# Performance work log

Measured on AMD Instinct MI355X. Metric: run time of the kernel, lower is better.

## Reference

```python
import jax, jax.numpy as jnp
import numpy as np

N = 8192
EPS = 1e-6


def setup_inputs() -> dict:
    key = jax.random.key(0)
    k1, k2, k3, k4 = jax.random.split(key, 4)
    P_risk = jax.random.normal(k1, (N,), dtype=jnp.float32)
    P_surv = jax.random.normal(k2, (N,), dtype=jnp.float32)
    T = jax.random.uniform(k3, (N,), dtype=jnp.float32)
    E = jax.random.randint(k4, (N,), 0, 2, dtype=jnp.int32)
    return {"P_risk": P_risk, "P_surv": P_surv, "T": T, "E": E}


def _compute_loss(P, M, E_eff):
    # P: [N] log-hazards, M: [N, N] float mask, E_eff: [N] effective event weights
    P_exp = jnp.exp(P)
    # sum_j M[i, j] * exp(P[j])  -- masked risk-set sum as a matvec
    P_exp_sum = M @ P_exp
    log_ratio = jnp.log(P_exp / (P_exp_sum + EPS))
    return -jnp.sum(log_ratio * E_eff) / jnp.sum(E_eff)


def reference(P_risk, P_surv, T, E):
    Ef = E.astype(jnp.float32)
    # M_risk[i, j] = 1 if T[i] < T[j]
    M_risk = (T[:, None] < T[None, :]).astype(jnp.float32)
    # M_surv[i, j] = 1 if T[i] > T[j] and E[j] == 1
    M_surv = (T[:, None] > T[None, :]).astype(jnp.float32) * Ef[None, :]

    # mode='risk': E * (row of M_risk nonempty)
    E_risk = Ef * (jnp.sum(M_risk, axis=1) > 0).astype(jnp.float32)
    # mode='surv': just (row of M_surv nonempty)
    E_surv = (jnp.sum(M_surv, axis=1) > 0).astype(jnp.float32)

    loss_risk = _compute_loss(P_risk, M_risk, E_risk)
    loss_surv = _compute_loss(P_surv, M_surv, E_surv)
    return (loss_risk, loss_surv)
```

## Files before the change

kernel.cpp:

```cpp
#include <hip/hip_runtime.h>
#include <math.h>

#define NN   8192
#define R    8
#define HALF (NN / 2)
#define GX   ((NN / R) * 2)

#define EPSF 1e-6f


__global__ __launch_bounds__(256, 8) void ds_main(
    const float* __restrict__ Pr, const float* __restrict__ Ps,
    const float* __restrict__ T,  const int* __restrict__ E,
    float* __restrict__ sumR0, float* __restrict__ sumR1,
    float* __restrict__ sumS0, float* __restrict__ sumS1) {
  const int tid   = threadIdx.x;
  const int g     = blockIdx.x >> 1;
  const int h     = blockIdx.x & 1;
  const int row0  = g * R;
  const int jbase = h * HALF;

  float Ti[R];
#pragma unroll
  for (int r = 0; r < R; ++r) Ti[r] = T[row0 + r];

  float sr[R], ss[R];
#pragma unroll
  for (int r = 0; r < R; ++r) { sr[r] = 0.0f; ss[r] = 0.0f; }

  for (int k = 0; k < HALF; k += 1024) {
    const int j = jbase + k + tid * 4;
    float4 t4  = *(const float4*)(T  + j);
    float4 pr4 = *(const float4*)(Pr + j);
    float4 ps4 = *(const float4*)(Ps + j);
    int4   e4  = *(const int4*)(E  + j);
    float er0 = __expf(pr4.x), er1 = __expf(pr4.y),
          er2 = __expf(pr4.z), er3 = __expf(pr4.w);
    float es0 = e4.x ? __expf(ps4.x) : 0.0f;
    float es1 = e4.y ? __expf(ps4.y) : 0.0f;
    float es2 = e4.z ? __expf(ps4.z) : 0.0f;
    float es3 = e4.w ? __expf(ps4.w) : 0.0f;
#pragma unroll
    for (int r = 0; r < R; ++r) {
      bool g0 = t4.x > Ti[r];  sr[r] += g0 ? er0 : 0.0f;  ss[r] += g0 ? 0.0f : es0;
      bool g1 = t4.y > Ti[r];  sr[r] += g1 ? er1 : 0.0f;  ss[r] += g1 ? 0.0f : es1;
      bool g2 = t4.z > Ti[r];  sr[r] += g2 ? er2 : 0.0f;  ss[r] += g2 ? 0.0f : es2;
      bool g3 = t4.w > Ti[r];  sr[r] += g3 ? er3 : 0.0f;  ss[r] += g3 ? 0.0f : es3;
    }
  }

#pragma unroll
  for (int r = 0; r < R; ++r) {
    for (int off = 32; off > 0; off >>= 1) {
      sr[r] += __shfl_down(sr[r], off);
      ss[r] += __shfl_down(ss[r], off);
    }
  }
  __shared__ float sh[4][2 * R];
  const int wid = tid >> 6, lane = tid & 63;
  if (lane == 0) {
#pragma unroll
    for (int r = 0; r < R; ++r) { sh[wid][r] = sr[r]; sh[wid][R + r] = ss[r]; }
  }
  __syncthreads();
  if (tid < 2 * R) {
    float v = sh[0][tid] + sh[1][tid] + sh[2][tid] + sh[3][tid];
    float* SR = h ? sumR1 : sumR0;
    float* SS = h ? sumS1 : sumS0;
    if (tid < R) SR[row0 + tid] = v;
    else         SS[row0 + (tid - R)] = v;
  }
}

__global__ __launch_bounds__(1024) void ds_finalize(
    const float* __restrict__ Pr, const float* __restrict__ Ps,
    const int* __restrict__ E,
    const float* __restrict__ sumR0, const float* __restrict__ sumR1,
    const float* __restrict__ sumS0, const float* __restrict__ sumS1,
    float* __restrict__ out) {
  float nr = 0.0f, dr = 0.0f, ns = 0.0f, nds = 0.0f;
  for (int i = threadIdx.x; i < NN; i += 1024) {
    const int e = E[i];
    const float prv = Pr[i], psv = Ps[i];
    const float es_diag = e ? __expf(psv) : 0.0f;
    const float srv = sumR0[i] + sumR1[i];
    const float ssv = (sumS0[i] + sumS1[i]) - es_diag;
    const float wr  = (e != 0 && srv > 0.0f) ? 1.0f : 0.0f;
    const float wsv = (ssv > 0.0f) ? 1.0f : 0.0f;
    nr  += wr  * (prv - logf(srv + EPSF));
    dr  += wr;
    ns  += wsv * (psv - logf(ssv + EPSF));
    nds += wsv;
  }
  for (int off = 32; off > 0; off >>= 1) {
    nr  += __shfl_down(nr,  off);
    dr  += __shfl_down(dr,  off);
    ns  += __shfl_down(ns,  off);
    nds += __shfl_down(nds, off);
  }
  __shared__ float sh[4][16];
  const int wid = threadIdx.x >> 6, lane = threadIdx.x & 63;
  if (lane == 0) {
    sh[0][wid] = nr; sh[1][wid] = dr; sh[2][wid] = ns; sh[3][wid] = nds;
  }
  __syncthreads();
  if (threadIdx.x == 0) {
    float NR = 0, DR = 0, NS = 0, DS = 0;
#pragma unroll
    for (int w = 0; w < 16; ++w) {
      NR += sh[0][w]; DR += sh[1][w]; NS += sh[2][w]; DS += sh[3][w];
    }
    out[0] = -NR / DR;
    out[1] = -NS / DS;
  }
}

extern "C" void kernel_launch(void* const* d_in, const int* in_sizes, int n_in,
                              void* d_out, int out_size, void* d_ws, size_t ws_size,
                              hipStream_t stream) {
  const float* Pr = (const float*)d_in[0];
  const float* Ps = (const float*)d_in[1];
  const float* T  = (const float*)d_in[2];
  const int*   E  = (const int*)d_in[3];
  float* out = (float*)d_out;

  float* ws    = (float*)d_ws;
  float* sumR0 = ws;
  float* sumR1 = ws + NN;
  float* sumS0 = ws + 2 * NN;
  float* sumS1 = ws + 3 * NN;

  ds_main<<<GX, 256, 0, stream>>>(Pr, Ps, T, E, sumR0, sumR1, sumS0, sumS1);
  ds_finalize<<<1, 1024, 0, stream>>>(Pr, Ps, E, sumR0, sumR1, sumS0, sumS1, out);
}
```

Before: 75.96 us.

## Precompute packed exp values in bf16 with a prep kernel, drop the column split

Adds a prep kernel that computes exp(P_risk) and the E-masked exp(P_surv) once per element and packs them as two bf16 values next to T in an 8-byte record. The main kernel then reads one packed stream per column instead of four arrays and no longer recomputes exponentials for every row block. The grid is also changed from two half-column blocks per row group to one full-column block, which removes the partial-sum merge. This adds a kernel launch and rounds the exponentials to bf16, which loses precision in the risk-set sums.

Measured after the change: 76.47 us. Within noise of the previous version (+0.7%).

```diff
diff --git a/kernel.cpp b/kernel.cpp
--- a/kernel.cpp
+++ b/kernel.cpp
@@ -3,22 +3,33 @@
 
 #define NN   8192
 #define R    8
-#define HALF (NN / 2)
-#define GX   ((NN / R) * 2)
-
+#define GX   (NN / R)
 #define EPSF 1e-6f
 
 
-__global__ __launch_bounds__(256, 8) void ds_main(
+__device__ __forceinline__ unsigned bf16_rne(float x) {
+  unsigned u = __float_as_uint(x);
+  u += 0x7fffu + ((u >> 16) & 1u);
+  return u >> 16;
+}
+
+__global__ __launch_bounds__(256) void ds_prep(
     const float* __restrict__ Pr, const float* __restrict__ Ps,
     const float* __restrict__ T,  const int* __restrict__ E,
-    float* __restrict__ sumR0, float* __restrict__ sumR1,
-    float* __restrict__ sumS0, float* __restrict__ sumS1) {
-  const int tid   = threadIdx.x;
-  const int g     = blockIdx.x >> 1;
-  const int h     = blockIdx.x & 1;
-  const int row0  = g * R;
-  const int jbase = h * HALF;
+    uint2* __restrict__ pack2) {
+  int i = blockIdx.x * 256 + threadIdx.x;
+  float t  = T[i];
+  float er = __expf(Pr[i]);
+  float es = E[i] ? __expf(Ps[i]) : 0.0f;
+  unsigned c = bf16_rne(er) | (bf16_rne(es) << 16);
+  pack2[i] = make_uint2(__float_as_uint(t), c);
+}
+
+__global__ __launch_bounds__(256, 4) void ds_main(
+    const float* __restrict__ T, const int4* __restrict__ pack2,
+    float* __restrict__ sumR, float* __restrict__ sumS) {
+  const int tid  = threadIdx.x;
+  const int row0 = blockIdx.x * R;
 
   float Ti[R];
 #pragma unroll
@@ -28,24 +39,31 @@
 #pragma unroll
   for (int r = 0; r < R; ++r) { sr[r] = 0.0f; ss[r] = 0.0f; }
 
-  for (int k = 0; k < HALF; k += 1024) {
-    const int j = jbase + k + tid * 4;
-    float4 t4  = *(const float4*)(T  + j);
-    float4 pr4 = *(const float4*)(Pr + j);
-    float4 ps4 = *(const float4*)(Ps + j);
-    int4   e4  = *(const int4*)(E  + j);
-    float er0 = __expf(pr4.x), er1 = __expf(pr4.y),
-          er2 = __expf(pr4.z), er3 = __expf(pr4.w);
-    float es0 = e4.x ? __expf(ps4.x) : 0.0f;
-    float es1 = e4.y ? __expf(ps4.y) : 0.0f;
-    float es2 = e4.z ? __expf(ps4.z) : 0.0f;
-    float es3 = e4.w ? __expf(ps4.w) : 0.0f;
 #pragma unroll
-    for (int r = 0; r < R; ++r) {
-      bool g0 = t4.x > Ti[r];  sr[r] += g0 ? er0 : 0.0f;  ss[r] += g0 ? 0.0f : es0;
-      bool g1 = t4.y > Ti[r];  sr[r] += g1 ? er1 : 0.0f;  ss[r] += g1 ? 0.0f : es1;
-      bool g2 = t4.z > Ti[r];  sr[r] += g2 ? er2 : 0.0f;  ss[r] += g2 ? 0.0f : es2;
-      bool g3 = t4.w > Ti[r];  sr[r] += g3 ? er3 : 0.0f;  ss[r] += g3 ? 0.0f : es3;
+  for (int it = 0; it < 4; ++it) {
+    const int m = it * 1024 + tid;
+    int4 q0 = pack2[m];
+    int4 q1 = pack2[m + 256];
+    int4 q2 = pack2[m + 512];
+    int4 q3 = pack2[m + 768];
+#pragma unroll
+    for (int q = 0; q < 4; ++q) {
+      int4 p = (q == 0) ? q0 : (q == 1) ? q1 : (q == 2) ? q2 : q3;
+      float    t0 = __int_as_float(p.x);
+      unsigned c0 = (unsigned)p.y;
+      float    er0 = __uint_as_float(c0 << 16);
+      float    es0 = __uint_as_float(c0 & 0xffff0000u);
+      float    t1 = __int_as_float(p.z);
+      unsigned c1 = (unsigned)p.w;
+      float    er1 = __uint_as_float(c1 << 16);
+      float    es1 = __uint_as_float(c1 & 0xffff0000u);
+#pragma unroll
+      for (int r = 0; r < R; ++r) {
+        bool g0 = t0 > Ti[r];
+        sr[r] += g0 ? er0 : 0.0f;   ss[r] += g0 ? 0.0f : es0;
+        bool g1 = t1 > Ti[r];
+        sr[r] += g1 ? er1 : 0.0f;   ss[r] += g1 ? 0.0f : es1;
+      }
     }
   }
 
@@ -65,26 +83,23 @@
   __syncthreads();
   if (tid < 2 * R) {
     float v = sh[0][tid] + sh[1][tid] + sh[2][tid] + sh[3][tid];
-    float* SR = h ? sumR1 : sumR0;
-    float* SS = h ? sumS1 : sumS0;
-    if (tid < R) SR[row0 + tid] = v;
-    else         SS[row0 + (tid - R)] = v;
+    if (tid < R) sumR[row0 + tid] = v;
+    else         sumS[row0 + (tid - R)] = v;
   }
 }
 
 __global__ __launch_bounds__(1024) void ds_finalize(
     const float* __restrict__ Pr, const float* __restrict__ Ps,
-    const int* __restrict__ E,
-    const float* __restrict__ sumR0, const float* __restrict__ sumR1,
-    const float* __restrict__ sumS0, const float* __restrict__ sumS1,
+    const int* __restrict__ E,    const uint2* __restrict__ pack2,
+    const float* __restrict__ sumR, const float* __restrict__ sumS,
     float* __restrict__ out) {
   float nr = 0.0f, dr = 0.0f, ns = 0.0f, nds = 0.0f;
   for (int i = threadIdx.x; i < NN; i += 1024) {
     const int e = E[i];
     const float prv = Pr[i], psv = Ps[i];
-    const float es_diag = e ? __expf(psv) : 0.0f;
-    const float srv = sumR0[i] + sumR1[i];
-    const float ssv = (sumS0[i] + sumS1[i]) - es_diag;
+    const float es_diag = __uint_as_float(pack2[i].y & 0xffff0000u);
+    const float srv = sumR[i];
+    const float ssv = sumS[i] - es_diag;
     const float wr  = (e != 0 && srv > 0.0f) ? 1.0f : 0.0f;
     const float wsv = (ssv > 0.0f) ? 1.0f : 0.0f;
     nr  += wr  * (prv - logf(srv + EPSF));
@@ -124,12 +139,12 @@
   const int*   E  = (const int*)d_in[3];
   float* out = (float*)d_out;
 
-  float* ws    = (float*)d_ws;
-  float* sumR0 = ws;
-  float* sumR1 = ws + NN;
-  float* sumS0 = ws + 2 * NN;
-  float* sumS1 = ws + 3 * NN;
+  char*  ws    = (char*)d_ws;
+  uint2* pack2 = (uint2*)ws;
+  float* sumR  = (float*)(ws + (size_t)NN * sizeof(uint2));
+  float* sumS  = sumR + NN;
 
-  ds_main<<<GX, 256, 0, stream>>>(Pr, Ps, T, E, sumR0, sumR1, sumS0, sumS1);
-  ds_finalize<<<1, 1024, 0, stream>>>(Pr, Ps, E, sumR0, sumR1, sumS0, sumS1, out);
+  ds_prep<<<NN / 256, 256, 0, stream>>>(Pr, Ps, T, E, pack2);
+  ds_main<<<GX, 256, 0, stream>>>(T, (const int4*)pack2, sumR, sumS);
+  ds_finalize<<<1, 1024, 0, stream>>>(Pr, Ps, E, pack2, sumR, sumS, out);
 }
```

## Compute masks with scaled med3 clamp, derive surv sum by complement, drop column split

Applied to the files above, without the earlier changes.

The compare-and-select masks are replaced by a med3 clamp of the scaled time difference (T*2^30), so each mask costs a subtract plus med3 and feeds FMA accumulation. The survival sum is now the total event-weighted exp sum minus the accumulated above-threshold part, with clamping to zero in finalize. The column halving across blocks is removed: each block covers all columns with software-prefetched float4 loads and a per-wave staggered start, and the launch bound drops from 8 to 4 blocks per CU. Risks include the clamp being exactly 0 or 1 only when time differences exceed 2^-30, cancellation error in the complement subtraction, and half as many blocks to fill the GPU.

New measurement: 86.29 us. 13.6% more time.

```diff
diff --git a/kernel.cpp b/kernel.cpp
--- a/kernel.cpp
+++ b/kernel.cpp
@@ -3,88 +3,108 @@
 
 #define NN   8192
 #define R    8
-#define HALF (NN / 2)
-#define GX   ((NN / R) * 2)
-
+#define GX   (NN / R)
 #define EPSF 1e-6f
+#define BIGF 1073741824.0f
 
 
-__global__ __launch_bounds__(256, 8) void ds_main(
+__global__ __launch_bounds__(256, 4) void ds_main(
     const float* __restrict__ Pr, const float* __restrict__ Ps,
     const float* __restrict__ T,  const int* __restrict__ E,
-    float* __restrict__ sumR0, float* __restrict__ sumR1,
-    float* __restrict__ sumS0, float* __restrict__ sumS1) {
-  const int tid   = threadIdx.x;
-  const int g     = blockIdx.x >> 1;
-  const int h     = blockIdx.x & 1;
-  const int row0  = g * R;
-  const int jbase = h * HALF;
+    float* __restrict__ sumR, float* __restrict__ sumS) {
+  const int tid  = threadIdx.x;
+  const int wid  = tid >> 6, lane = tid & 63;
+  const int row0 = blockIdx.x * R;
 
-  float Ti[R];
+  float TiB[R];
 #pragma unroll
-  for (int r = 0; r < R; ++r) Ti[r] = T[row0 + r];
+  for (int r = 0; r < R; ++r) TiB[r] = T[row0 + r] * BIGF;
 
-  float sr[R], ss[R];
+  float sr[R], sa[R];
 #pragma unroll
-  for (int r = 0; r < R; ++r) { sr[r] = 0.0f; ss[r] = 0.0f; }
+  for (int r = 0; r < R; ++r) { sr[r] = 0.0f; sa[r] = 0.0f; }
+  float tot = 0.0f;
 
-  for (int k = 0; k < HALF; k += 1024) {
-    const int j = jbase + k + tid * 4;
-    float4 t4  = *(const float4*)(T  + j);
-    float4 pr4 = *(const float4*)(Pr + j);
-    float4 ps4 = *(const float4*)(Ps + j);
-    int4   e4  = *(const int4*)(E  + j);
-    float er0 = __expf(pr4.x), er1 = __expf(pr4.y),
-          er2 = __expf(pr4.z), er3 = __expf(pr4.w);
-    float es0 = e4.x ? __expf(ps4.x) : 0.0f;
-    float es1 = e4.y ? __expf(ps4.y) : 0.0f;
-    float es2 = e4.z ? __expf(ps4.z) : 0.0f;
-    float es3 = e4.w ? __expf(ps4.w) : 0.0f;
+  const float4* T4  = (const float4*)T;
+  const float4* Pr4 = (const float4*)Pr;
+  const float4* Ps4 = (const float4*)Ps;
+  const int4*   E4  = (const int4*)E;
+
+  const int c0 = (2 * wid) & 7;
+  int m = c0 * 256 + tid;
+  float4 t4 = T4[m], pr4 = Pr4[m], ps4 = Ps4[m];
+  int4   e4 = E4[m];
+
+#pragma unroll
+  for (int it = 0; it < 8; ++it) {
+    const int cn = (it + 1 + 2 * wid) & 7;
+    const int mn = cn * 256 + tid;
+    float4 t4n = T4[mn], pr4n = Pr4[mn], ps4n = Ps4[mn];
+    int4   e4n = E4[mn];
+
+    const float tB0 = t4.x * BIGF, tB1 = t4.y * BIGF,
+                tB2 = t4.z * BIGF, tB3 = t4.w * BIGF;
+    const float er0 = __expf(pr4.x), er1 = __expf(pr4.y),
+                er2 = __expf(pr4.z), er3 = __expf(pr4.w);
+    const float es0 = e4.x ? __expf(ps4.x) : 0.0f;
+    const float es1 = e4.y ? __expf(ps4.y) : 0.0f;
+    const float es2 = e4.z ? __expf(ps4.z) : 0.0f;
+    const float es3 = e4.w ? __expf(ps4.w) : 0.0f;
+    tot += (es0 + es1) + (es2 + es3);
+
 #pragma unroll
     for (int r = 0; r < R; ++r) {
-      bool g0 = t4.x > Ti[r];  sr[r] += g0 ? er0 : 0.0f;  ss[r] += g0 ? 0.0f : es0;
-      bool g1 = t4.y > Ti[r];  sr[r] += g1 ? er1 : 0.0f;  ss[r] += g1 ? 0.0f : es1;
-      bool g2 = t4.z > Ti[r];  sr[r] += g2 ? er2 : 0.0f;  ss[r] += g2 ? 0.0f : es2;
-      bool g3 = t4.w > Ti[r];  sr[r] += g3 ? er3 : 0.0f;  ss[r] += g3 ? 0.0f : es3;
+      const float m0 = __builtin_amdgcn_fmed3f(tB0 - TiB[r], 0.0f, 1.0f);
+      const float m1 = __builtin_amdgcn_fmed3f(tB1 - TiB[r], 0.0f, 1.0f);
+      const float m2 = __builtin_amdgcn_fmed3f(tB2 - TiB[r], 0.0f, 1.0f);
+      const float m3 = __builtin_amdgcn_fmed3f(tB3 - TiB[r], 0.0f, 1.0f);
+      sr[r] = fmaf(m0, er0, sr[r]);  sa[r] = fmaf(m0, es0, sa[r]);
+      sr[r] = fmaf(m1, er1, sr[r]);  sa[r] = fmaf(m1, es1, sa[r]);
+      sr[r] = fmaf(m2, er2, sr[r]);  sa[r] = fmaf(m2, es2, sa[r]);
+      sr[r] = fmaf(m3, er3, sr[r]);  sa[r] = fmaf(m3, es3, sa[r]);
     }
+    t4 = t4n; pr4 = pr4n; ps4 = ps4n; e4 = e4n;
   }
 
 #pragma unroll
   for (int r = 0; r < R; ++r) {
     for (int off = 32; off > 0; off >>= 1) {
       sr[r] += __shfl_down(sr[r], off);
-      ss[r] += __shfl_down(ss[r], off);
+      sa[r] += __shfl_down(sa[r], off);
     }
   }
-  __shared__ float sh[4][2 * R];
-  const int wid = tid >> 6, lane = tid & 63;
+  for (int off = 32; off > 0; off >>= 1) tot += __shfl_down(tot, off);
+
+  __shared__ float sh[4][2 * R + 1];
   if (lane == 0) {
 #pragma unroll
-    for (int r = 0; r < R; ++r) { sh[wid][r] = sr[r]; sh[wid][R + r] = ss[r]; }
+    for (int r = 0; r < R; ++r) { sh[wid][r] = sr[r]; sh[wid][R + r] = sa[r]; }
+    sh[wid][2 * R] = tot;
   }
   __syncthreads();
   if (tid < 2 * R) {
-    float v = sh[0][tid] + sh[1][tid] + sh[2][tid] + sh[3][tid];
-    float* SR = h ? sumR1 : sumR0;
-    float* SS = h ? sumS1 : sumS0;
-    if (tid < R) SR[row0 + tid] = v;
-    else         SS[row0 + (tid - R)] = v;
+    const float v  = sh[0][tid] + sh[1][tid] + sh[2][tid] + sh[3][tid];
+    if (tid < R) {
+      sumR[row0 + tid] = v;
+    } else {
+      const float tT = sh[0][2 * R] + sh[1][2 * R] + sh[2][2 * R] + sh[3][2 * R];
+      sumS[row0 + (tid - R)] = tT - v;
+    }
   }
 }
 
 __global__ __launch_bounds__(1024) void ds_finalize(
     const float* __restrict__ Pr, const float* __restrict__ Ps,
     const int* __restrict__ E,
-    const float* __restrict__ sumR0, const float* __restrict__ sumR1,
-    const float* __restrict__ sumS0, const float* __restrict__ sumS1,
+    const float* __restrict__ sumR, const float* __restrict__ sumS,
     float* __restrict__ out) {
   float nr = 0.0f, dr = 0.0f, ns = 0.0f, nds = 0.0f;
   for (int i = threadIdx.x; i < NN; i += 1024) {
     const int e = E[i];
     const float prv = Pr[i], psv = Ps[i];
     const float es_diag = e ? __expf(psv) : 0.0f;
-    const float srv = sumR0[i] + sumR1[i];
-    const float ssv = (sumS0[i] + sumS1[i]) - es_diag;
+    const float srv = fmaxf(sumR[i], 0.0f);
+    const float ssv = fmaxf(sumS[i] - es_diag, 0.0f);
     const float wr  = (e != 0 && srv > 0.0f) ? 1.0f : 0.0f;
     const float wsv = (ssv > 0.0f) ? 1.0f : 0.0f;
     nr  += wr  * (prv - logf(srv + EPSF));
@@ -124,12 +144,9 @@
   const int*   E  = (const int*)d_in[3];
   float* out = (float*)d_out;
 
-  float* ws    = (float*)d_ws;
-  float* sumR0 = ws;
-  float* sumR1 = ws + NN;
-  float* sumS0 = ws + 2 * NN;
-  float* sumS1 = ws + 3 * NN;
+  float* sumR = (float*)d_ws;
+  float* sumS = sumR + NN;
 
-  ds_main<<<GX, 256, 0, stream>>>(Pr, Ps, T, E, sumR0, sumR1, sumS0, sumS1);
-  ds_finalize<<<1, 1024, 0, stream>>>(Pr, Ps, E, sumR0, sumR1, sumS0, sumS1, out);
+  ds_main<<<GX, 256, 0, stream>>>(Pr, Ps, T, E, sumR, sumS);
+  ds_finalize<<<1, 1024, 0, stream>>>(Pr, Ps, E, sumR, sumS, out);
 }
```
